# Performance work log

Hardware: AMD Instinct MI355X
Metric: run time of the kernel (lower is better)

## Reference

```python
import jax, jax.numpy as jnp
from jax import lax
import numpy as np

H_AA = 20          # raw Potts alphabet
H_PAD = 22         # after (0,2) pad on both residue axes
EMB = H_PAD * H_PAD  # 484, LightAttention channel dim == MLP width
KSZ = 9            # LightAttention conv kernel


def setup_inputs() -> dict:
    key = jax.random.key(0)
    ks = jax.random.split(key, 16)
    b, n, k = 8, 512, 30
    S_mut = 99
    sc = 0.02
    inp = {
        'batch_etab': jax.random.normal(ks[0], (b, n, k, H_AA * H_AA), dtype=jnp.float32),
        'E_idx': jax.random.randint(ks[1], (b, n, k), 0, n),
        'sortcery_seqs': jax.random.randint(ks[2], (b, S_mut, n), 0, H_AA),
        'seqs': jax.random.randint(ks[3], (b, n), 0, H_AA),
        'mut_pos': jax.random.randint(ks[4], (b,), 0, n),
        'nodes': jnp.zeros((1,), dtype=jnp.float32),
        # LightAttention params (Conv1d: [out_ch, in_ch, ksz])
        'W_f': jax.random.normal(ks[5], (EMB, EMB, KSZ), dtype=jnp.float32) * sc,
        'b_f': jnp.zeros((EMB,), dtype=jnp.float32),
        'W_a': jax.random.normal(ks[6], (EMB, EMB, KSZ), dtype=jnp.float32) * sc,
        'b_a': jnp.zeros((EMB,), dtype=jnp.float32),
        # both_out: ReLU -> Linear(EMB,EMB) -> ReLU -> Linear(EMB,484)
        'W1': jax.random.normal(ks[7], (EMB, EMB), dtype=jnp.float32) * sc,
        'b1': jnp.zeros((EMB,), dtype=jnp.float32),
        'W2': jax.random.normal(ks[8], (EMB, EMB), dtype=jnp.float32) * sc,
        'b2': jnp.zeros((EMB,), dtype=jnp.float32),
        # ddg_out: Linear(1,1) -> scalar affine
        'w_ddg': jax.random.normal(ks[9], (1, 1), dtype=jnp.float32),
        'b_ddg': jnp.zeros((1,), dtype=jnp.float32),
    }
    return inp


def _conv1d_same(x, W, b):
    # x: [B, C, L], W: [O, I, K] -> [B, O, L] (stride 1, SAME pad for K=9)
    p = KSZ // 2
    y = lax.conv_general_dilated(x, W, (1,), [(p, p)],
                                 dimension_numbers=('NCH', 'OIH', 'NCH'))
    return y + b[None, :, None]


def reference(batch_etab, E_idx, sortcery_seqs, seqs, mut_pos, nodes,
              W_f, b_f, W_a, b_a, W1, b1, W2, b2, w_ddg, b_ddg):
    b, n, k, hh = batch_etab.shape
    h = H_AA
    # view (b,n,k,h,h), pad last two dims (0,2) each, flatten -> (b,n,k,484)
    e = batch_etab.reshape(b, n, k, h, h)
    e = jnp.pad(e, ((0, 0), (0, 0), (0, 0), (0, 2), (0, 2)))
    e = e.reshape(b, n, k, EMB)

    bidx = jnp.arange(b)
    # expand_etab_4d followed by [mut_pos] row-select == scatter the mut_pos
    # neighbor slab into a dense [n, EMB] row (avoids the full [n,n,EMB] dense).
    rows = e[bidx, mut_pos]          # [b, k, EMB]
    nbrs = E_idx[bidx, mut_pos]      # [b, k]
    lin = jnp.zeros((b, n, EMB), dtype=batch_etab.dtype)
    lin = lin.at[bidx[:, None], nbrs].set(rows)   # [b, n, EMB]

    mask = lin[:, :, 0] != 0                       # [b, n]

    # LightAttention (eval mode: dropout = identity)
    x = lin.transpose(0, 2, 1)                     # [b, EMB, n]
    o = _conv1d_same(x, W_f, b_f)
    att = _conv1d_same(x, W_a, b_a)
    att = jnp.where(mask[:, None, :], att, -1e9)
    o1 = o * jax.nn.softmax(att, axis=-1)          # [b, EMB, n]
    la = o1.transpose(0, 2, 1)                     # [b, n, EMB]

    # both_out: ReLU -> Linear -> ReLU -> Linear
    y = jax.nn.relu(la) @ W1.T + b1
    y = jax.nn.relu(y) @ W2.T + b2                 # [b, n, 484]
    # ddg_out Linear(1,1) applied elementwise on trailing singleton
    ddg = y * w_ddg[0, 0] + b_ddg[0]               # [b, n, 484]

    etab2 = ddg.reshape(b, n, H_PAD, H_PAD)        # [b, n, 22, 22]

    sort_seqs = jnp.concatenate([sortcery_seqs, seqs[:, None, :]], axis=1)  # [b,S,n]
    S = sort_seqs.shape[1]
    # batch_score_seq_batch_pos: score[b,s] = sum_j etab2[b, j, seq[mut_pos], seq[j]]
    s_pos = jnp.take_along_axis(sort_seqs, mut_pos[:, None, None], axis=2)[..., 0]  # [b,S]
    scores = etab2[bidx[:, None, None], jnp.arange(n)[None, None, :],
                   s_pos[:, :, None], sort_seqs].sum(axis=-1)  # [b, S]

    # subtract WT (last) score, drop WT row
    all_scores = (scores - scores[:, -1:])[:, :-1]             # [b, S-1]
    return all_scores
```

## Files before the change

kernel.cpp:

```cpp
#include <hip/hip_runtime.h>
#include <math.h>

#define H_AA   20
#define H_PAD  22
#define EMB    484
#define KSZ    9
#define NB     8
#define NPOS   512
#define KNBR   30
#define SMUT   99
#define STOT   100
#define MAXPAIR 288
#define ROWS   (NB*KNBR)

__global__ void setup_kernel(const int* __restrict__ E_idx,
                             const int* __restrict__ mut_pos,
                             const float* __restrict__ etab,
                             int* __restrict__ jmap_g,
                             int* __restrict__ rowidx_g,
                             int* __restrict__ mcount,
                             int* __restrict__ pairs,
                             int* __restrict__ npairs) {
    int b  = blockIdx.x;
    int mp = mut_pos[b];
    __shared__ int jmap[NPOS];
    __shared__ int wcnt[8], wbase[8];
    __shared__ int paircnt;
    int t = threadIdx.x;
    jmap[t] = -1;
    if (t == 0) paircnt = 0;
    __syncthreads();
    if (t < KNBR) {
        int nb = E_idx[(b * NPOS + mp) * KNBR + t];
        bool winner = true;
        for (int j2 = t + 1; j2 < KNBR; ++j2)
            if (E_idx[(b * NPOS + mp) * KNBR + j2] == nb) { winner = false; break; }
        if (winner) jmap[nb] = t;
    }
    __syncthreads();
    int j = jmap[t];
    int f = 0;
    if (j >= 0) {
        float c0 = etab[(((size_t)(b * NPOS + mp)) * KNBR + j) * 400];
        f = (c0 != 0.0f) ? 1 : 0;
    }
    jmap_g[b * NPOS + t] = j;
    unsigned long long bal = __ballot(f);
    int lane = t & 63, w = t >> 6;
    if (lane == 0) wcnt[w] = __popcll(bal);
    __syncthreads();
    if (t == 0) {
        int s = 0;
        for (int ww = 0; ww < 8; ++ww) { wbase[ww] = s; s += wcnt[ww]; }
        mcount[b] = s;
    }
    __syncthreads();
    int ridx = -1;
    if (f) ridx = wbase[w] + __popcll(bal & ((1ull << lane) - 1ull));
    rowidx_g[b * NPOS + t] = ridx;
    if (f) {
        for (int d = -4; d <= 4; ++d) {
            int q = t + d;
            if (q < 0 || q >= NPOS) continue;
            int jq = jmap[q];
            if (jq < 0) continue;
            int idx = atomicAdd(&paircnt, 1);
            pairs[b * MAXPAIR + idx] = (ridx << 10) | ((d + 4) << 5) | jq;
        }
    }
    __syncthreads();
    if (t == 0) npairs[b] = paircnt;
}

#define TDIM 32
__global__ void transpose_kernel(const float* __restrict__ src,
                                 float* __restrict__ dst, int R, int C) {
    __shared__ float tile[TDIM][TDIM + 1];
    int c0 = blockIdx.x * TDIM;
    int r0 = blockIdx.y * TDIM;
    for (int ty = threadIdx.y; ty < TDIM; ty += blockDim.y) {
        int r = r0 + ty, c = c0 + threadIdx.x;
        if (r < R && c < C) tile[ty][threadIdx.x] = src[(size_t)r * C + c];
    }
    __syncthreads();
    for (int ty = threadIdx.y; ty < TDIM; ty += blockDim.y) {
        int c = c0 + ty, r = r0 + threadIdx.x;
        if (r < R && c < C) dst[(size_t)c * R + r] = tile[threadIdx.x][ty];
    }
}

__global__ void init_oa_kernel(const float* __restrict__ b_f,
                               const float* __restrict__ b_a,
                               double* __restrict__ o_d,
                               double* __restrict__ a_d) {
    int idx = blockIdx.x * blockDim.x + threadIdx.x;
    const int N = ROWS * EMB;
    if (idx < N)            o_d[idx]     = (double)b_f[idx % EMB];
    else if (idx < 2 * N)   a_d[idx - N] = (double)b_a[(idx - N) % EMB];
}

__global__ void conv_pair_kernel(const float* __restrict__ etab,
                                 const float* __restrict__ Wtf,
                                 const float* __restrict__ Wta,
                                 const int* __restrict__ mut_pos,
                                 const int* __restrict__ pairs,
                                 const int* __restrict__ npairs,
                                 double* __restrict__ o_d,
                                 double* __restrict__ a_d) {
    int b    = blockIdx.x / MAXPAIR;
    int pidx = blockIdx.x % MAXPAIR;
    if (pidx >= npairs[b]) return;
    int pk  = pairs[b * MAXPAIR + pidx];
    int i   = pk >> 10;
    int tap = (pk >> 5) & 31;
    int j   = pk & 31;
    int mp  = mut_pos[b];
    __shared__ float xs[400];
    int t = threadIdx.x;
    const float* src = etab + (((size_t)(b * NPOS + mp)) * KNBR + j) * 400;
    for (int u = t; u < 400; u += 256) xs[u] = src[u];
    __syncthreads();
    int half = t >> 7, c4 = t & 127;
    if (c4 >= 121) return;
    const float* W = half ? Wta : Wtf;
    double a0 = 0, a1 = 0, a2 = 0, a3 = 0;
    for (int r = 0; r < H_AA; ++r) {
        #pragma unroll 4
        for (int cc = 0; cc < H_AA; ++cc) {
            int in = r * H_PAD + cc;
            float4 wv = *(reinterpret_cast<const float4*>(
                              W + (size_t)(in * KSZ + tap) * EMB) + c4);
            float xv = xs[r * H_AA + cc];
            a0 += (double)wv.x * xv; a1 += (double)wv.y * xv;
            a2 += (double)wv.z * xv; a3 += (double)wv.w * xv;
        }
    }
    double* dst = (half ? a_d : o_d) + ((size_t)(b * KNBR + i)) * EMB + c4 * 4;
    atomicAdd(dst + 0, a0); atomicAdd(dst + 1, a1);
    atomicAdd(dst + 2, a2); atomicAdd(dst + 3, a3);
}

__global__ void softmax_kernel(const double* __restrict__ o_d,
                               const double* __restrict__ a_d,
                               const int* __restrict__ mcount,
                               float* __restrict__ la) {
    int idx = blockIdx.x * blockDim.x + threadIdx.x;
    if (idx >= NB * EMB) return;
    int b = idx / EMB, ch = idx % EMB;
    int m = mcount[b];
    float mx = -1e30f;
    for (int i = 0; i < m; ++i)
        mx = fmaxf(mx, (float)a_d[((size_t)(b * KNBR + i)) * EMB + ch]);
    double sum = 0.0;
    for (int i = 0; i < m; ++i)
        sum += (double)expf((float)a_d[((size_t)(b * KNBR + i)) * EMB + ch] - mx);
    for (int i = 0; i < m; ++i) {
        size_t o = ((size_t)(b * KNBR + i)) * EMB + ch;
        float w = (float)((double)expf((float)a_d[o] - mx) / sum);
        la[o] = (float)o_d[o] * w;
    }
}

__global__ void mlp_kernel(const float* __restrict__ la,
                           const float* __restrict__ W1t,
                           const float* __restrict__ b1,
                           const float* __restrict__ W2t,
                           const float* __restrict__ b2,
                           const float* __restrict__ w_ddg,
                           const float* __restrict__ b_ddg,
                           const int* __restrict__ mcount,
                           float* __restrict__ rows_out,
                           float* __restrict__ bg) {
    __shared__ float  xs[EMB];
    __shared__ double red[4 * EMB];
    int blk  = blockIdx.x;
    bool isbg = (blk == ROWS);
    int b = blk / KNBR, i = blk % KNBR;
    if (!isbg && i >= mcount[b]) return;
    int t  = threadIdx.x;
    int q  = t >> 7, c4 = t & 127;
    for (int u = t; u < EMB; u += 512)
        xs[u] = isbg ? 0.0f : fmaxf(la[((size_t)(b * KNBR + i)) * EMB + u], 0.0f);
    __syncthreads();
    if (c4 < 121) {
        double a0 = 0, a1 = 0, a2 = 0, a3 = 0;
        int u0 = q * 121;
        #pragma unroll 4
        for (int u = u0; u < u0 + 121; ++u) {
            float4 wv = *(reinterpret_cast<const float4*>(W1t + (size_t)u * EMB) + c4);
            float xv = xs[u];
            a0 += (double)wv.x * xv; a1 += (double)wv.y * xv;
            a2 += (double)wv.z * xv; a3 += (double)wv.w * xv;
        }
        red[q * EMB + c4 * 4 + 0] = a0; red[q * EMB + c4 * 4 + 1] = a1;
        red[q * EMB + c4 * 4 + 2] = a2; red[q * EMB + c4 * 4 + 3] = a3;
    }
    __syncthreads();
    float y1f = 0.0f;
    if (t < EMB) {
        double y = (double)b1[t] + red[t] + red[EMB + t] + red[2 * EMB + t] + red[3 * EMB + t];
        y1f = fmaxf((float)y, 0.0f);
    }
    __syncthreads();
    if (t < EMB) xs[t] = y1f;
    __syncthreads();
    if (c4 < 121) {
        double a0 = 0, a1 = 0, a2 = 0, a3 = 0;
        int u0 = q * 121;
        #pragma unroll 4
        for (int u = u0; u < u0 + 121; ++u) {
            float4 wv = *(reinterpret_cast<const float4*>(W2t + (size_t)u * EMB) + c4);
            float xv = xs[u];
            a0 += (double)wv.x * xv; a1 += (double)wv.y * xv;
            a2 += (double)wv.z * xv; a3 += (double)wv.w * xv;
        }
        red[q * EMB + c4 * 4 + 0] = a0; red[q * EMB + c4 * 4 + 1] = a1;
        red[q * EMB + c4 * 4 + 2] = a2; red[q * EMB + c4 * 4 + 3] = a3;
    }
    __syncthreads();
    if (t < EMB) {
        double y = (double)b2[t] + red[t] + red[EMB + t] + red[2 * EMB + t] + red[3 * EMB + t];
        float dd = (float)y * w_ddg[0] + b_ddg[0];
        if (isbg) bg[t] = dd;
        else      rows_out[((size_t)(b * KNBR + i)) * EMB + t] = dd;
    }
}

__global__ void score_kernel(const int* __restrict__ sortc,
                             const int* __restrict__ seqs,
                             const int* __restrict__ mut_pos,
                             const int* __restrict__ rowidx,
                             const float* __restrict__ rows,
                             const float* __restrict__ bg,
                             double* __restrict__ scoresD) {
    int blk = blockIdx.x;
    int b = blk / STOT, s = blk % STOT;
    int mp = mut_pos[b];
    int a = (s < SMUT) ? sortc[((size_t)b * SMUT + s) * NPOS + mp]
                       : seqs[b * NPOS + mp];
    int lane = threadIdx.x;
    double acc = 0.0;
    for (int j = lane; j < NPOS; j += 64) {
        int c = (s < SMUT) ? sortc[((size_t)b * SMUT + s) * NPOS + j]
                           : seqs[b * NPOS + j];
        int i = rowidx[b * NPOS + j];
        float v = (i >= 0) ? rows[((size_t)(b * KNBR + i)) * EMB + a * H_PAD + c]
                           : bg[a * H_PAD + c];
        acc += (double)v;
    }
    for (int off = 32; off > 0; off >>= 1)
        acc += __shfl_down(acc, off, 64);
    if (lane == 0) scoresD[blk] = acc;
}

__global__ void final_kernel(const double* __restrict__ scoresD,
                             float* __restrict__ out) {
    int idx = blockIdx.x * blockDim.x + threadIdx.x;
    if (idx >= NB * SMUT) return;
    int b = idx / SMUT, s = idx % SMUT;
    out[idx] = (float)(scoresD[b * STOT + s] - scoresD[b * STOT + SMUT]);
}

extern "C" void kernel_launch(void* const* d_in, const int* in_sizes, int n_in,
                              void* d_out, int out_size, void* d_ws, size_t ws_size,
                              hipStream_t stream) {
    const float* etab = (const float*)d_in[0];
    const int*   E_idx = (const int*)d_in[1];
    const int*   sortc = (const int*)d_in[2];
    const int*   seqs  = (const int*)d_in[3];
    const int*   mutp  = (const int*)d_in[4];
    const float* W_f = (const float*)d_in[6];
    const float* b_f = (const float*)d_in[7];
    const float* W_a = (const float*)d_in[8];
    const float* b_a = (const float*)d_in[9];
    const float* W1  = (const float*)d_in[10];
    const float* b1  = (const float*)d_in[11];
    const float* W2  = (const float*)d_in[12];
    const float* b2  = (const float*)d_in[13];
    const float* wdd = (const float*)d_in[14];
    const float* bdd = (const float*)d_in[15];
    float* out = (float*)d_out;

    char* wsb = (char*)d_ws;
    size_t off = 0;
    auto alloc = [&](size_t bytes) -> void* {
        void* p = wsb + off;
        off = (off + bytes + 255) & ~((size_t)255);
        return p;
    };
    float*  Wtf     = (float*)alloc((size_t)EMB * EMB * KSZ * 4);
    float*  Wta     = (float*)alloc((size_t)EMB * EMB * KSZ * 4);
    float*  W1t     = (float*)alloc((size_t)EMB * EMB * 4);
    float*  W2t     = (float*)alloc((size_t)EMB * EMB * 4);
    int*    jmap    = (int*)alloc((size_t)NB * NPOS * 4);
    int*    rowidx  = (int*)alloc((size_t)NB * NPOS * 4);
    int*    mcount  = (int*)alloc((size_t)NB * 4);
    int*    pairs   = (int*)alloc((size_t)NB * MAXPAIR * 4);
    int*    npairs  = (int*)alloc((size_t)NB * 4);
    double* o_d     = (double*)alloc((size_t)ROWS * EMB * 8);
    double* a_d     = (double*)alloc((size_t)ROWS * EMB * 8);
    float*  la_buf  = (float*)alloc((size_t)ROWS * EMB * 4);
    float*  rows    = (float*)alloc((size_t)ROWS * EMB * 4);
    float*  bg      = (float*)alloc((size_t)EMB * 4);
    double* scoresD = (double*)alloc((size_t)NB * STOT * 8);
    (void)ws_size; (void)in_sizes; (void)n_in; (void)out_size;

    setup_kernel<<<NB, 512, 0, stream>>>(E_idx, mutp, etab, jmap, rowidx,
                                         mcount, pairs, npairs);

    dim3 tb(TDIM, 8);
    {
        dim3 g((EMB * KSZ + TDIM - 1) / TDIM, (EMB + TDIM - 1) / TDIM);
        transpose_kernel<<<g, tb, 0, stream>>>(W_f, Wtf, EMB, EMB * KSZ);
        transpose_kernel<<<g, tb, 0, stream>>>(W_a, Wta, EMB, EMB * KSZ);
    }
    {
        dim3 g((EMB + TDIM - 1) / TDIM, (EMB + TDIM - 1) / TDIM);
        transpose_kernel<<<g, tb, 0, stream>>>(W1, W1t, EMB, EMB);
        transpose_kernel<<<g, tb, 0, stream>>>(W2, W2t, EMB, EMB);
    }

    init_oa_kernel<<<(2 * ROWS * EMB + 255) / 256, 256, 0, stream>>>(b_f, b_a, o_d, a_d);
    conv_pair_kernel<<<NB * MAXPAIR, 256, 0, stream>>>(etab, Wtf, Wta, mutp,
                                                       pairs, npairs, o_d, a_d);
    softmax_kernel<<<(NB * EMB + 255) / 256, 256, 0, stream>>>(o_d, a_d, mcount, la_buf);
    mlp_kernel<<<ROWS + 1, 512, 0, stream>>>(la_buf, W1t, b1, W2t, b2, wdd, bdd,
                                             mcount, rows, bg);
    score_kernel<<<NB * STOT, 64, 0, stream>>>(sortc, seqs, mutp, rowidx, rows, bg, scoresD);
    final_kernel<<<(NB * SMUT + 255) / 256, 256, 0, stream>>>(scoresD, out);
}
```

Baseline: 418.6 us.

## Restructure conv and MLP as tiled per-tap GEMMs with packed weights

Replaces the per-pair conv kernel, which streamed the full weight slice for every (row,tap,neighbor) pair, with a tap-grouped tiled GEMM. Pairs with the same tap share weight tiles from a packed weight matrix that holds only the 400 non-pad input channels and stacks the feature and attention halves together. The per-row MLP kernel becomes two tiled GEMM launches over all rows, with the background row folded in as an extra zero row. Buffer init moves to a memset, and bias is added on tap 4. This cuts redundant weight traffic at the cost of more launches and fp64 atomics spread across tiles.

```diff
diff --git a/kernel.cpp b/kernel.cpp
--- a/kernel.cpp
+++ b/kernel.cpp
@@ -10,25 +10,24 @@
 #define KNBR   30
 #define SMUT   99
 #define STOT   100
-#define MAXPAIR 288
 #define ROWS   (NB*KNBR)
+#define MROWS  241
+#define NTOT   968
+#define KC     400
 
 __global__ void setup_kernel(const int* __restrict__ E_idx,
                              const int* __restrict__ mut_pos,
                              const float* __restrict__ etab,
-                             int* __restrict__ jmap_g,
                              int* __restrict__ rowidx_g,
                              int* __restrict__ mcount,
-                             int* __restrict__ pairs,
-                             int* __restrict__ npairs) {
+                             int* __restrict__ pairtap,
+                             int* __restrict__ cnttap) {
     int b  = blockIdx.x;
     int mp = mut_pos[b];
     __shared__ int jmap[NPOS];
     __shared__ int wcnt[8], wbase[8];
-    __shared__ int paircnt;
     int t = threadIdx.x;
     jmap[t] = -1;
-    if (t == 0) paircnt = 0;
     __syncthreads();
     if (t < KNBR) {
         int nb = E_idx[(b * NPOS + mp) * KNBR + t];
@@ -44,7 +43,6 @@
         float c0 = etab[(((size_t)(b * NPOS + mp)) * KNBR + j) * 400];
         f = (c0 != 0.0f) ? 1 : 0;
     }
-    jmap_g[b * NPOS + t] = j;
     unsigned long long bal = __ballot(f);
     int lane = t & 63, w = t >> 6;
     if (lane == 0) wcnt[w] = __popcll(bal);
@@ -59,170 +57,229 @@
     if (f) ridx = wbase[w] + __popcll(bal & ((1ull << lane) - 1ull));
     rowidx_g[b * NPOS + t] = ridx;
     if (f) {
+        int row = b * KNBR + ridx;
         for (int d = -4; d <= 4; ++d) {
             int q = t + d;
             if (q < 0 || q >= NPOS) continue;
             int jq = jmap[q];
             if (jq < 0) continue;
-            int idx = atomicAdd(&paircnt, 1);
-            pairs[b * MAXPAIR + idx] = (ridx << 10) | ((d + 4) << 5) | jq;
-        }
-    }
-    __syncthreads();
-    if (t == 0) npairs[b] = paircnt;
-}
-
-#define TDIM 32
-__global__ void transpose_kernel(const float* __restrict__ src,
-                                 float* __restrict__ dst, int R, int C) {
-    __shared__ float tile[TDIM][TDIM + 1];
-    int c0 = blockIdx.x * TDIM;
-    int r0 = blockIdx.y * TDIM;
-    for (int ty = threadIdx.y; ty < TDIM; ty += blockDim.y) {
+            int tap = d + 4;
+            int idx = atomicAdd(&cnttap[tap], 1);
+            pairtap[tap * 256 + idx] = (row << 5) | jq;
+        }
+    }
+}
+
+__global__ void pack_conv_kernel(const float* __restrict__ Wf,
+                                 const float* __restrict__ Wa,
+                                 float* __restrict__ Wp) {
+    int half = blockIdx.z;
+    const float* src = half ? Wa : Wf;
+    int cb = blockIdx.x * 32;
+    int ob = blockIdx.y * 32;
+    __shared__ float tile[32][33];
+    for (int yy = threadIdx.y; yy < 32; yy += 8) {
+        int out = ob + yy, c = cb + threadIdx.x;
+        if (out < EMB && c < EMB * KSZ)
+            tile[yy][threadIdx.x] = src[(size_t)out * (EMB * KSZ) + c];
+    }
+    __syncthreads();
+    for (int yy = threadIdx.y; yy < 32; yy += 8) {
+        int c = cb + yy, out = ob + threadIdx.x;
+        if (c < EMB * KSZ && out < EMB) {
+            int tap = c % 9, in_pad = c / 9;
+            int rr = in_pad / H_PAD, cc = in_pad % H_PAD;
+            if (rr < H_AA && cc < H_AA) {
+                int k = tap * KC + rr * H_AA + cc;
+                Wp[(size_t)k * NTOT + half * EMB + out] = tile[threadIdx.x][yy];
+            }
+        }
+    }
+}
+
+__global__ void transpose_lin_kernel(const float* __restrict__ W1,
+                                     const float* __restrict__ W2,
+                                     float* __restrict__ W1t,
+                                     float* __restrict__ W2t) {
+    const float* src = blockIdx.z ? W2 : W1;
+    float*       dst = blockIdx.z ? W2t : W1t;
+    __shared__ float tile[32][33];
+    int c0 = blockIdx.x * 32, r0 = blockIdx.y * 32;
+    for (int ty = threadIdx.y; ty < 32; ty += 8) {
         int r = r0 + ty, c = c0 + threadIdx.x;
-        if (r < R && c < C) tile[ty][threadIdx.x] = src[(size_t)r * C + c];
-    }
-    __syncthreads();
-    for (int ty = threadIdx.y; ty < TDIM; ty += blockDim.y) {
+        if (r < EMB && c < EMB) tile[ty][threadIdx.x] = src[(size_t)r * EMB + c];
+    }
+    __syncthreads();
+    for (int ty = threadIdx.y; ty < 32; ty += 8) {
         int c = c0 + ty, r = r0 + threadIdx.x;
-        if (r < R && c < C) dst[(size_t)c * R + r] = tile[threadIdx.x][ty];
-    }
-}
-
-__global__ void init_oa_kernel(const float* __restrict__ b_f,
-                               const float* __restrict__ b_a,
-                               double* __restrict__ o_d,
-                               double* __restrict__ a_d) {
-    int idx = blockIdx.x * blockDim.x + threadIdx.x;
-    const int N = ROWS * EMB;
-    if (idx < N)            o_d[idx]     = (double)b_f[idx % EMB];
-    else if (idx < 2 * N)   a_d[idx - N] = (double)b_a[(idx - N) % EMB];
-}
-
-__global__ void conv_pair_kernel(const float* __restrict__ etab,
-                                 const float* __restrict__ Wtf,
-                                 const float* __restrict__ Wta,
+        if (r < EMB && c < EMB) dst[(size_t)c * EMB + r] = tile[threadIdx.x][ty];
+    }
+}
+
+__global__ void conv_gemm_kernel(const float* __restrict__ etab,
+                                 const float* __restrict__ Wp,
+                                 const float* __restrict__ b_f,
+                                 const float* __restrict__ b_a,
                                  const int* __restrict__ mut_pos,
-                                 const int* __restrict__ pairs,
-                                 const int* __restrict__ npairs,
-                                 double* __restrict__ o_d,
-                                 double* __restrict__ a_d) {
-    int b    = blockIdx.x / MAXPAIR;
-    int pidx = blockIdx.x % MAXPAIR;
-    if (pidx >= npairs[b]) return;
-    int pk  = pairs[b * MAXPAIR + pidx];
-    int i   = pk >> 10;
-    int tap = (pk >> 5) & 31;
-    int j   = pk & 31;
-    int mp  = mut_pos[b];
-    __shared__ float xs[400];
+                                 const int* __restrict__ pairtap,
+                                 const int* __restrict__ cnttap,
+                                 double* __restrict__ C) {
+    int tap   = blockIdx.x / 15;
+    int chunk = blockIdx.x % 15;
+    int cnt = cnttap[tap];
+    if (chunk * 16 >= cnt) return;
+    int nt0 = blockIdx.y * 64;
     int t = threadIdx.x;
-    const float* src = etab + (((size_t)(b * NPOS + mp)) * KNBR + j) * 400;
-    for (int u = t; u < 400; u += 256) xs[u] = src[u];
-    __syncthreads();
-    int half = t >> 7, c4 = t & 127;
-    if (c4 >= 121) return;
-    const float* W = half ? Wta : Wtf;
-    double a0 = 0, a1 = 0, a2 = 0, a3 = 0;
-    for (int r = 0; r < H_AA; ++r) {
-        #pragma unroll 4
-        for (int cc = 0; cc < H_AA; ++cc) {
-            int in = r * H_PAD + cc;
-            float4 wv = *(reinterpret_cast<const float4*>(
-                              W + (size_t)(in * KSZ + tap) * EMB) + c4);
-            float xv = xs[r * H_AA + cc];
-            a0 += (double)wv.x * xv; a1 += (double)wv.y * xv;
-            a2 += (double)wv.z * xv; a3 += (double)wv.w * xv;
-        }
-    }
-    double* dst = (half ? a_d : o_d) + ((size_t)(b * KNBR + i)) * EMB + c4 * 4;
-    atomicAdd(dst + 0, a0); atomicAdd(dst + 1, a1);
-    atomicAdd(dst + 2, a2); atomicAdd(dst + 3, a3);
-}
-
-__global__ void softmax_kernel(const double* __restrict__ o_d,
-                               const double* __restrict__ a_d,
+    int g = t >> 6, nl = t & 63;
+    int n = nt0 + nl;
+
+    __shared__ int   prow[16];
+    __shared__ int   pbase[16];
+    __shared__ float Ws[16][64];
+    __shared__ float Xs[16][20];
+
+    if (t < 16) {
+        int idx = chunk * 16 + t;
+        int pk = (idx < cnt) ? pairtap[tap * 256 + idx] : -1;
+        int row = pk >> 5;
+        prow[t] = (pk >= 0) ? row : -1;
+        if (pk >= 0) {
+            int b = row / KNBR;
+            pbase[t] = ((b * NPOS + mut_pos[b]) * KNBR + (pk & 31)) * 400;
+        } else pbase[t] = 0;
+    }
+
+    double binit = 0.0;
+    if (tap == 4 && n < NTOT)
+        binit = (double)(n < EMB ? b_f[n] : b_a[n - EMB]);
+    double a0 = binit, a1 = binit, a2 = binit, a3 = binit;
+    __syncthreads();
+
+    int kkl = t >> 4, c4 = t & 15;
+    for (int kb = 0; kb < KC; kb += 16) {
+        {
+            int nc = nt0 + c4 * 4;
+            const float* wrow = Wp + (size_t)(tap * KC + kb + kkl) * NTOT;
+            float4 w = make_float4(0.f, 0.f, 0.f, 0.f);
+            if (nc + 3 < NTOT) w = *(const float4*)(wrow + nc);
+            else {
+                if (nc     < NTOT) w.x = wrow[nc];
+                if (nc + 1 < NTOT) w.y = wrow[nc + 1];
+                if (nc + 2 < NTOT) w.z = wrow[nc + 2];
+            }
+            *(float4*)&Ws[kkl][c4 * 4] = w;
+        }
+        {
+            int m = t >> 4, kk = t & 15;
+            int row = prow[m];
+            float xv = 0.0f;
+            if (row >= 0) xv = etab[(size_t)pbase[m] + kb + kk];
+            Xs[kk][m] = xv;
+        }
+        __syncthreads();
+        #pragma unroll
+        for (int kk = 0; kk < 16; ++kk) {
+            double w = (double)Ws[kk][nl];
+            float4 x4 = *(const float4*)&Xs[kk][g * 4];
+            a0 += w * (double)x4.x;
+            a1 += w * (double)x4.y;
+            a2 += w * (double)x4.z;
+            a3 += w * (double)x4.w;
+        }
+        __syncthreads();
+    }
+    if (n < NTOT) {
+        int r0 = prow[g * 4 + 0], r1 = prow[g * 4 + 1];
+        int r2 = prow[g * 4 + 2], r3 = prow[g * 4 + 3];
+        if (r0 >= 0) atomicAdd(&C[(size_t)r0 * NTOT + n], a0);
+        if (r1 >= 0) atomicAdd(&C[(size_t)r1 * NTOT + n], a1);
+        if (r2 >= 0) atomicAdd(&C[(size_t)r2 * NTOT + n], a2);
+        if (r3 >= 0) atomicAdd(&C[(size_t)r3 * NTOT + n], a3);
+    }
+}
+
+__global__ void softmax_kernel(const double* __restrict__ C,
                                const int* __restrict__ mcount,
                                float* __restrict__ la) {
     int idx = blockIdx.x * blockDim.x + threadIdx.x;
     if (idx >= NB * EMB) return;
     int b = idx / EMB, ch = idx % EMB;
     int m = mcount[b];
+    if (m == 0) return;
     float mx = -1e30f;
     for (int i = 0; i < m; ++i)
-        mx = fmaxf(mx, (float)a_d[((size_t)(b * KNBR + i)) * EMB + ch]);
+        mx = fmaxf(mx, (float)C[(size_t)(b * KNBR + i) * NTOT + EMB + ch]);
     double sum = 0.0;
     for (int i = 0; i < m; ++i)
-        sum += (double)expf((float)a_d[((size_t)(b * KNBR + i)) * EMB + ch] - mx);
+        sum += (double)expf((float)C[(size_t)(b * KNBR + i) * NTOT + EMB + ch] - mx);
     for (int i = 0; i < m; ++i) {
-        size_t o = ((size_t)(b * KNBR + i)) * EMB + ch;
-        float w = (float)((double)expf((float)a_d[o] - mx) / sum);
-        la[o] = (float)o_d[o] * w;
-    }
-}
-
-__global__ void mlp_kernel(const float* __restrict__ la,
-                           const float* __restrict__ W1t,
-                           const float* __restrict__ b1,
-                           const float* __restrict__ W2t,
-                           const float* __restrict__ b2,
-                           const float* __restrict__ w_ddg,
-                           const float* __restrict__ b_ddg,
-                           const int* __restrict__ mcount,
-                           float* __restrict__ rows_out,
-                           float* __restrict__ bg) {
-    __shared__ float  xs[EMB];
-    __shared__ double red[4 * EMB];
-    int blk  = blockIdx.x;
-    bool isbg = (blk == ROWS);
-    int b = blk / KNBR, i = blk % KNBR;
-    if (!isbg && i >= mcount[b]) return;
-    int t  = threadIdx.x;
-    int q  = t >> 7, c4 = t & 127;
-    for (int u = t; u < EMB; u += 512)
-        xs[u] = isbg ? 0.0f : fmaxf(la[((size_t)(b * KNBR + i)) * EMB + u], 0.0f);
-    __syncthreads();
-    if (c4 < 121) {
-        double a0 = 0, a1 = 0, a2 = 0, a3 = 0;
-        int u0 = q * 121;
-        #pragma unroll 4
-        for (int u = u0; u < u0 + 121; ++u) {
-            float4 wv = *(reinterpret_cast<const float4*>(W1t + (size_t)u * EMB) + c4);
-            float xv = xs[u];
-            a0 += (double)wv.x * xv; a1 += (double)wv.y * xv;
-            a2 += (double)wv.z * xv; a3 += (double)wv.w * xv;
-        }
-        red[q * EMB + c4 * 4 + 0] = a0; red[q * EMB + c4 * 4 + 1] = a1;
-        red[q * EMB + c4 * 4 + 2] = a2; red[q * EMB + c4 * 4 + 3] = a3;
-    }
-    __syncthreads();
-    float y1f = 0.0f;
-    if (t < EMB) {
-        double y = (double)b1[t] + red[t] + red[EMB + t] + red[2 * EMB + t] + red[3 * EMB + t];
-        y1f = fmaxf((float)y, 0.0f);
-    }
-    __syncthreads();
-    if (t < EMB) xs[t] = y1f;
-    __syncthreads();
-    if (c4 < 121) {
-        double a0 = 0, a1 = 0, a2 = 0, a3 = 0;
-        int u0 = q * 121;
-        #pragma unroll 4
-        for (int u = u0; u < u0 + 121; ++u) {
-            float4 wv = *(reinterpret_cast<const float4*>(W2t + (size_t)u * EMB) + c4);
-            float xv = xs[u];
-            a0 += (double)wv.x * xv; a1 += (double)wv.y * xv;
-            a2 += (double)wv.z * xv; a3 += (double)wv.w * xv;
-        }
-        red[q * EMB + c4 * 4 + 0] = a0; red[q * EMB + c4 * 4 + 1] = a1;
-        red[q * EMB + c4 * 4 + 2] = a2; red[q * EMB + c4 * 4 + 3] = a3;
-    }
-    __syncthreads();
-    if (t < EMB) {
-        double y = (double)b2[t] + red[t] + red[EMB + t] + red[2 * EMB + t] + red[3 * EMB + t];
-        float dd = (float)y * w_ddg[0] + b_ddg[0];
-        if (isbg) bg[t] = dd;
-        else      rows_out[((size_t)(b * KNBR + i)) * EMB + t] = dd;
+        size_t o = (size_t)(b * KNBR + i) * NTOT;
+        float w = (float)((double)expf((float)C[o + EMB + ch] - mx) / sum);
+        la[(size_t)(b * KNBR + i) * EMB + ch] = (float)C[o + ch] * w;
+    }
+}
+
+__global__ void mlp_gemm_kernel(const float* __restrict__ X,
+                                const float* __restrict__ Wt,
+                                const float* __restrict__ bias,
+                                const float* __restrict__ wdd,
+                                const float* __restrict__ bdd,
+                                float* __restrict__ Y, int mode) {
+    int m0  = blockIdx.x * 16;
+    int nt0 = blockIdx.y * 64;
+    int t = threadIdx.x;
+    int g = t >> 6, nl = t & 63;
+    int n = nt0 + nl;
+    __shared__ float Ws[16][64];
+    __shared__ float Xs[16][20];
+    double a0 = 0, a1 = 0, a2 = 0, a3 = 0;
+    int kkl = t >> 4, c4 = t & 15;
+    for (int kb = 0; kb < EMB; kb += 16) {
+        {
+            int k = kb + kkl;
+            int nc = nt0 + c4 * 4;
+            float4 w = make_float4(0.f, 0.f, 0.f, 0.f);
+            if (k < EMB) {
+                const float* wrow = Wt + (size_t)k * EMB;
+                if (nc + 3 < EMB) w = *(const float4*)(wrow + nc);
+                else {
+                    if (nc     < EMB) w.x = wrow[nc];
+                    if (nc + 1 < EMB) w.y = wrow[nc + 1];
+                    if (nc + 2 < EMB) w.z = wrow[nc + 2];
+                }
+            }
+            *(float4*)&Ws[kkl][c4 * 4] = w;
+        }
+        {
+            int m = t >> 4, kk = t & 15;
+            int row = m0 + m, k = kb + kk;
+            float xv = 0.0f;
+            if (row < MROWS && k < EMB)
+                xv = fmaxf(X[(size_t)row * EMB + k], 0.0f);
+            Xs[kk][m] = xv;
+        }
+        __syncthreads();
+        #pragma unroll
+        for (int kk = 0; kk < 16; ++kk) {
+            double w = (double)Ws[kk][nl];
+            float4 x4 = *(const float4*)&Xs[kk][g * 4];
+            a0 += w * (double)x4.x;
+            a1 += w * (double)x4.y;
+            a2 += w * (double)x4.z;
+            a3 += w * (double)x4.w;
+        }
+        __syncthreads();
+    }
+    if (n < EMB) {
+        double bs = (double)bias[n];
+        double acc[4] = {a0, a1, a2, a3};
+        for (int r = 0; r < 4; ++r) {
+            int row = m0 + g * 4 + r;
+            if (row >= MROWS) continue;
+            float v = (float)(acc[r] + bs);
+            if (mode == 2) v = v * wdd[0] + bdd[0];
+            Y[(size_t)row * EMB + n] = v;
+        }
     }
 }
 
@@ -230,27 +287,28 @@
                              const int* __restrict__ seqs,
                              const int* __restrict__ mut_pos,
                              const int* __restrict__ rowidx,
-                             const float* __restrict__ rows,
-                             const float* __restrict__ bg,
+                             const float* __restrict__ rows_all,
                              double* __restrict__ scoresD) {
     int blk = blockIdx.x;
     int b = blk / STOT, s = blk % STOT;
     int mp = mut_pos[b];
     int a = (s < SMUT) ? sortc[((size_t)b * SMUT + s) * NPOS + mp]
                        : seqs[b * NPOS + mp];
-    int lane = threadIdx.x;
+    int t = threadIdx.x;
     double acc = 0.0;
-    for (int j = lane; j < NPOS; j += 64) {
+    for (int j = t; j < NPOS; j += 256) {
         int c = (s < SMUT) ? sortc[((size_t)b * SMUT + s) * NPOS + j]
                            : seqs[b * NPOS + j];
         int i = rowidx[b * NPOS + j];
-        float v = (i >= 0) ? rows[((size_t)(b * KNBR + i)) * EMB + a * H_PAD + c]
-                           : bg[a * H_PAD + c];
-        acc += (double)v;
-    }
+        int row = (i >= 0) ? (b * KNBR + i) : (ROWS);
+        acc += (double)rows_all[(size_t)row * EMB + a * H_PAD + c];
+    }
+    __shared__ double part[4];
     for (int off = 32; off > 0; off >>= 1)
         acc += __shfl_down(acc, off, 64);
-    if (lane == 0) scoresD[blk] = acc;
+    if ((t & 63) == 0) part[t >> 6] = acc;
+    __syncthreads();
+    if (t == 0) scoresD[blk] = part[0] + part[1] + part[2] + part[3];
 }
 
 __global__ void final_kernel(const double* __restrict__ scoresD,
@@ -288,44 +346,43 @@
         off = (off + bytes + 255) & ~((size_t)255);
         return p;
     };
-    float*  Wtf     = (float*)alloc((size_t)EMB * EMB * KSZ * 4);
-    float*  Wta     = (float*)alloc((size_t)EMB * EMB * KSZ * 4);
+    double* C       = (double*)alloc((size_t)ROWS * NTOT * 8);
+    float*  la_buf  = (float*)alloc((size_t)MROWS * EMB * 4);
+    int*    cnttap  = (int*)alloc(9 * 4);
+    size_t zbytes = off;
+    float*  Wp      = (float*)alloc((size_t)9 * KC * NTOT * 4);
     float*  W1t     = (float*)alloc((size_t)EMB * EMB * 4);
     float*  W2t     = (float*)alloc((size_t)EMB * EMB * 4);
-    int*    jmap    = (int*)alloc((size_t)NB * NPOS * 4);
     int*    rowidx  = (int*)alloc((size_t)NB * NPOS * 4);
     int*    mcount  = (int*)alloc((size_t)NB * 4);
-    int*    pairs   = (int*)alloc((size_t)NB * MAXPAIR * 4);
-    int*    npairs  = (int*)alloc((size_t)NB * 4);
-    double* o_d     = (double*)alloc((size_t)ROWS * EMB * 8);
-    double* a_d     = (double*)alloc((size_t)ROWS * EMB * 8);
-    float*  la_buf  = (float*)alloc((size_t)ROWS * EMB * 4);
-    float*  rows    = (float*)alloc((size_t)ROWS * EMB * 4);
-    float*  bg      = (float*)alloc((size_t)EMB * 4);
+    int*    pairtap = (int*)alloc((size_t)9 * 256 * 4);
+    float*  y1      = (float*)alloc((size_t)MROWS * EMB * 4);
+    float*  rows_all= (float*)alloc((size_t)MROWS * EMB * 4);
     double* scoresD = (double*)alloc((size_t)NB * STOT * 8);
     (void)ws_size; (void)in_sizes; (void)n_in; (void)out_size;
 
-    setup_kernel<<<NB, 512, 0, stream>>>(E_idx, mutp, etab, jmap, rowidx,
-                                         mcount, pairs, npairs);
-
-    dim3 tb(TDIM, 8);
+    hipMemsetAsync(d_ws, 0, zbytes, stream);
+
+    setup_kernel<<<NB, 512, 0, stream>>>(E_idx, mutp, etab, rowidx, mcount,
+                                         pairtap, cnttap);
+
     {
-        dim3 g((EMB * KSZ + TDIM - 1) / TDIM, (EMB + TDIM - 1) / TDIM);
-        transpose_kernel<<<g, tb, 0, stream>>>(W_f, Wtf, EMB, EMB * KSZ);
-        transpose_kernel<<<g, tb, 0, stream>>>(W_a, Wta, EMB, EMB * KSZ);
+        dim3 g((EMB * KSZ + 31) / 32, (EMB + 31) / 32, 2);
+        pack_conv_kernel<<<g, dim3(32, 8), 0, stream>>>(W_f, W_a, Wp);
     }
     {
-        dim3 g((EMB + TDIM - 1) / TDIM, (EMB + TDIM - 1) / TDIM);
-        transpose_kernel<<<g, tb, 0, stream>>>(W1, W1t, EMB, EMB);
-        transpose_kernel<<<g, tb, 0, stream>>>(W2, W2t, EMB, EMB);
-    }
-
-    init_oa_kernel<<<(2 * ROWS * EMB + 255) / 256, 256, 0, stream>>>(b_f, b_a, o_d, a_d);
-    conv_pair_kernel<<<NB * MAXPAIR, 256, 0, stream>>>(etab, Wtf, Wta, mutp,
-                                                       pairs, npairs, o_d, a_d);
-    softmax_kernel<<<(NB * EMB + 255) / 256, 256, 0, stream>>>(o_d, a_d, mcount, la_buf);
-    mlp_kernel<<<ROWS + 1, 512, 0, stream>>>(la_buf, W1t, b1, W2t, b2, wdd, bdd,
-                                             mcount, rows, bg);
-    score_kernel<<<NB * STOT, 64, 0, stream>>>(sortc, seqs, mutp, rowidx, rows, bg, scoresD);
+        dim3 g((EMB + 31) / 32, (EMB + 31) / 32, 2);
+        transpose_lin_kernel<<<g, dim3(32, 8), 0, stream>>>(W1, W2, W1t, W2t);
+    }
+
+    conv_gemm_kernel<<<dim3(9 * 15, 16), 256, 0, stream>>>(etab, Wp, b_f, b_a,
+                                                           mutp, pairtap, cnttap, C);
+    softmax_kernel<<<(NB * EMB + 255) / 256, 256, 0, stream>>>(C, mcount, la_buf);
+    mlp_gemm_kernel<<<dim3((MROWS + 15) / 16, (EMB + 63) / 64), 256, 0, stream>>>(
+        la_buf, W1t, b1, wdd, bdd, y1, 1);
+    mlp_gemm_kernel<<<dim3((MROWS + 15) / 16, (EMB + 63) / 64), 256, 0, stream>>>(
+        y1, W2t, b2, wdd, bdd, rows_all, 2);
+    score_kernel<<<NB * STOT, 256, 0, stream>>>(sortc, seqs, mutp, rowidx,
+                                                rows_all, scoresD);
     final_kernel<<<(NB * SMUT + 255) / 256, 256, 0, stream>>>(scoresD, out);
 }
```

Result: no change. 424.8 us (+1.5%).
